# Kernel optimization log

Hardware: AMD Instinct MI355X
Metric: run time of the kernel (lower is better)

## Reference

```python
import jax, jax.numpy as jnp
import numpy as np

VOCAB = 78
EMBED = 8
HIDDEN = 256
BATCH = 512
SEQ = 512


def _lstm_layer(x, Wih, Whh, bih, bhh):
    # x: [B, T, in_dim]; Wih: [4H, in_dim]; Whh: [4H, H]
    B, T, _ = x.shape
    H = Whh.shape[1]
    # Precompute input projections for all timesteps: [T, B, 4H]
    xg = (jnp.einsum('bti,gi->btg', x, Wih) + bih + bhh).transpose(1, 0, 2)

    def step(carry, xg_t):
        h, c = carry
        gates = xg_t + h @ Whh.T  # [B, 4H]
        i, f, g, o = jnp.split(gates, 4, axis=-1)  # PyTorch gate order i,f,g,o
        i = jax.nn.sigmoid(i)
        f = jax.nn.sigmoid(f)
        g = jnp.tanh(g)
        o = jax.nn.sigmoid(o)
        c = f * c + i * g
        h = o * jnp.tanh(c)
        return (h, c), h

    h0 = jnp.zeros((B, H), dtype=x.dtype)
    c0 = jnp.zeros((B, H), dtype=x.dtype)
    (_, _), hs = jax.lax.scan(step, (h0, c0), xg)
    return hs.transpose(1, 0, 2)  # [B, T, H]


def setup_inputs() -> dict:
    key = jax.random.key(0)
    ks = jax.random.split(key, 12)
    k = 1.0 / np.sqrt(HIDDEN)
    u = lambda kk, shp, bound=k: jax.random.uniform(kk, shp, jnp.float32, -bound, bound)
    return {
        'x': jax.random.randint(ks[0], (BATCH, SEQ), 0, VOCAB),
        'E': jax.random.normal(ks[1], (VOCAB, EMBED), jnp.float32),
        'Wih0': u(ks[2], (4 * HIDDEN, EMBED)),
        'Whh0': u(ks[3], (4 * HIDDEN, HIDDEN)),
        'bih0': u(ks[4], (4 * HIDDEN,)),
        'bhh0': u(ks[5], (4 * HIDDEN,)),
        'Wih1': u(ks[6], (4 * HIDDEN, HIDDEN)),
        'Whh1': u(ks[7], (4 * HIDDEN, HIDDEN)),
        'bih1': u(ks[8], (4 * HIDDEN,)),
        'bhh1': u(ks[9], (4 * HIDDEN,)),
        'Wfc': u(ks[10], (VOCAB, HIDDEN)),
        'bfc': u(ks[11], (VOCAB,)),
    }


def reference(x, E, Wih0, Whh0, bih0, bhh0, Wih1, Whh1, bih1, bhh1, Wfc, bfc):
    E = E.at[0].set(0.0)  # padding_idx=0
    h = E[x]  # [B, T, EMBED]
    h = _lstm_layer(h, Wih0, Whh0, bih0, bhh0)
    # dropout=0.2 between layers is inactive in eval mode
    h = _lstm_layer(h, Wih1, Whh1, bih1, bhh1)
    return h[:, -1, :] @ Wfc.T + bfc  # [B, VOCAB]
```

## Files before the change

### kernel.cpp

```cpp
#include <hip/hip_runtime.h>
#include <hip/hip_bf16.h>

#define VOCAB 78
#define EMBED 8
#define HID 256
#define BATCH 512
#define SEQ 512
#define G4H 1024

#define GB 8
#define GH 16
#define BS 64
#define HS 16

typedef short bf16x8 __attribute__((ext_vector_type(8)));
typedef float f32x4 __attribute__((ext_vector_type(4)));
typedef unsigned long long u64;

#define OFF_WHH0 0
#define OFF_WIH1 (512*1024)
#define OFF_WHH1 (1024*1024)
#define OFF_XG0  (1536*1024)
#define OFF_B1   (OFF_XG0 + 320*1024)
#define OFF_XT   (OFF_B1 + 4096)
#define OFF_H0   (OFF_XT + 1024*1024)
#define OFF_H1   (OFF_H0 + 512*1024)
#define OFF_H1F  (OFF_H1 + 512*1024)
#define OFF_CNT  (OFF_H1F + 512*1024)
#define WS_NEED  (OFF_CNT + 1024)

__device__ __forceinline__ float sigm(float x){ return 1.f/(1.f + __expf(-x)); }
__device__ __forceinline__ float tanh_f(float x){
  float e = __expf(-2.f * fabsf(x));
  float r = (1.f - e) / (1.f + e);
  return copysignf(r, x);
}
__device__ __forceinline__ unsigned short f2b(float x){
  unsigned u = __float_as_uint(x);
  unsigned r = (u + 0x7FFFu + ((u >> 16) & 1u)) >> 16;
  return (unsigned short)r;
}

__global__ void prep(const int* __restrict__ x, const float* __restrict__ E,
                     const float* __restrict__ Wih0, const float* __restrict__ Whh0,
                     const float* __restrict__ bih0, const float* __restrict__ bhh0,
                     const float* __restrict__ Wih1, const float* __restrict__ Whh1,
                     const float* __restrict__ bih1, const float* __restrict__ bhh1,
                     unsigned char* __restrict__ ws)
{
  unsigned short* Whh0b = (unsigned short*)(ws + OFF_WHH0);
  unsigned short* Wih1b = (unsigned short*)(ws + OFF_WIH1);
  unsigned short* Whh1b = (unsigned short*)(ws + OFF_WHH1);
  float* xg0 = (float*)(ws + OFF_XG0);
  float* b1  = (float*)(ws + OFF_B1);
  int*   xT  = (int*)(ws + OFF_XT);

  long id = (long)blockIdx.x * 256 + threadIdx.x;
  const long NW = 1024L * 256;
  if (id < NW) { Whh0b[id] = f2b(Whh0[id]); return; }
  id -= NW;
  if (id < NW) { Wih1b[id] = f2b(Wih1[id]); return; }
  id -= NW;
  if (id < NW) { Whh1b[id] = f2b(Whh1[id]); return; }
  id -= NW;
  if (id < (long)VOCAB*G4H) {
    int v = (int)(id / G4H), row = (int)(id % G4H);
    float s = bih0[row] + bhh0[row];
    if (v != 0) {
      #pragma unroll
      for (int e = 0; e < EMBED; e++) s += E[v*EMBED + e] * Wih0[row*EMBED + e];
    }
    xg0[id] = s; return;
  }
  id -= (long)VOCAB*G4H;
  if (id < (long)SEQ*BATCH) {
    int t = (int)(id / BATCH), b = (int)(id % BATCH);
    xT[t*BATCH + b] = x[b*SEQ + t]; return;
  }
  id -= (long)SEQ*BATCH;
  if (id < G4H) { b1[id] = bih1[id] + bhh1[id]; return; }
  id -= G4H;
  if (id < 262144) { ((unsigned*)(ws + OFF_H0))[id] = 0u; return; }
  id -= 262144;
  if (id < 256) { ((unsigned*)(ws + OFF_CNT))[id] = 0u; }
}

__global__ __launch_bounds__(256, 1) void lstm_sync(unsigned char* __restrict__ ws)
{
  const unsigned short* Wg = (const unsigned short*)(ws + OFF_WHH0);
  const float* xg0 = (const float*)(ws + OFF_XG0);
  const float* b1  = (const float*)(ws + OFF_B1);
  const int*   xT  = (const int*)(ws + OFF_XT);
  unsigned short* h0g = (unsigned short*)(ws + OFF_H0);
  unsigned short* h1g = (unsigned short*)(ws + OFF_H1);
  float* h1f = (float*)(ws + OFF_H1F);

  __shared__ __align__(16) unsigned char smem[3*32768 + 64*48];
  unsigned char* wlds = smem;
  unsigned char* hb   = smem + 3*32768;

  const int tid = threadIdx.x;
  const int m = tid >> 6, l = tid & 63, lc = l & 15, lq = l >> 4;
  const int gb = blockIdx.x & 7, gh = blockIdx.x >> 3;
  const int B0 = gb * BS, J = gh * HS;
  const int brow0 = B0 + m*16;

  unsigned* cA = (unsigned*)(ws + OFF_CNT) + gb*16;
  unsigned* cB = cA + 1;

  for (int idx = tid; idx < 3*64*32; idx += 256) {
    int mat = idx >> 11;
    int rem = idx & 2047;
    int cw  = rem >> 5;
    int c16 = rem & 31;
    int g = cw >> 4, r16 = cw & 15;
    int grow = g*256 + J + r16;
    bf16x8 v = *(const bf16x8*)(Wg + (size_t)mat*262144 + (size_t)grow*256 + c16*8);
    *(bf16x8*)(wlds + mat*32768 + cw*512 + ((c16*16) ^ ((cw&7)<<4))) = v;
  }

  float bias1v[4];
  #pragma unroll
  for (int g = 0; g < 4; g++) bias1v[g] = b1[g*256 + J + lc];

  int wb[3][4];
  const int swz = (lc & 7) << 4;
  #pragma unroll
  for (int g = 0; g < 4; g++) {
    int cw = g*16 + lc;
    wb[0][g] = 0*32768 + cw*512;
    wb[1][g] = 1*32768 + cw*512;
    wb[2][g] = 2*32768 + cw*512;
  }
  __syncthreads();

  float c0[4] = {0,0,0,0}, c1[4] = {0,0,0,0};
  u64 xret = 0;

#define MM(acc, a, mat)                                                          \
  _Pragma("unroll") for (int kt = 0; kt < 8; kt++) {                             \
    _Pragma("unroll") for (int g = 0; g < 4; g++) {                              \
      bf16x8 bfr = *(const bf16x8*)(wlds + wb[mat][g] + ((kt*64 + lq*16) ^ swz));\
      acc[g] = __builtin_amdgcn_mfma_f32_16x16x32_bf16(a[kt], bfr, acc[g], 0,0,0);\
    } }

  #pragma unroll 1
  for (int k = 0; k <= SEQ; ++k) {
    const int pk = k & 1, pkm1 = pk ^ 1;

    __builtin_amdgcn_sched_barrier(0);
    asm volatile("" ::: "memory");

    bf16x8 a0[8];
    { const u64* hp = (const u64*)(h0g + (size_t)pkm1*131072 + (size_t)(brow0+lc)*256 + lq*8);
      #pragma unroll
      for (int kt = 0; kt < 8; kt++) {
        union { u64 q[2]; bf16x8 v; } u;
        u.q[0] = __hip_atomic_load(hp + kt*8 + 0, __ATOMIC_RELAXED, __HIP_MEMORY_SCOPE_SYSTEM);
        u.q[1] = __hip_atomic_load(hp + kt*8 + 1, __ATOMIC_RELAXED, __HIP_MEMORY_SCOPE_SYSTEM);
        a0[kt] = u.v;
      } }
    bf16x8 a1[8];
    if (k >= 1) {
      const u64* hp = (const u64*)(h1g + (size_t)pk*131072 + (size_t)(brow0+lc)*256 + lq*8);
      #pragma unroll
      for (int kt = 0; kt < 8; kt++) {
        union { u64 q[2]; bf16x8 v; } u;
        u.q[0] = __hip_atomic_load(hp + kt*8 + 0, __ATOMIC_RELAXED, __HIP_MEMORY_SCOPE_SYSTEM);
        u.q[1] = __hip_atomic_load(hp + kt*8 + 1, __ATOMIC_RELAXED, __HIP_MEMORY_SCOPE_SYSTEM);
        a1[kt] = u.v;
      }
    }

    if (k < SEQ) {
      float xg[4][4];
      #pragma unroll
      for (int r = 0; r < 4; r++) {
        int tok = xT[k*BATCH + brow0 + lq*4 + r];
        const float* tr = xg0 + (size_t)tok*G4H + J + lc;
        #pragma unroll
        for (int g = 0; g < 4; g++) xg[g][r] = tr[g*256];
      }
      f32x4 acc0[4] = {{0,0,0,0},{0,0,0,0},{0,0,0,0},{0,0,0,0}};
      MM(acc0, a0, 0);
      #pragma unroll
      for (int r = 0; r < 4; r++) {
        float gi = sigm (acc0[0][r] + xg[0][r]);
        float gf = sigm (acc0[1][r] + xg[1][r]);
        float gg = tanh_f(acc0[2][r] + xg[2][r]);
        float go = sigm (acc0[3][r] + xg[3][r]);
        float c = gf*c0[r] + gi*gg;  c0[r] = c;
        *(unsigned short*)(hb + (m*16 + lq*4 + r)*48 + lc*2) = f2b(go * tanh_f(c));
      }
      __syncthreads();
      { u64 pv = *(const u64*)(hb + (tid>>2)*48 + (tid&3)*8);
        u64* dp = (u64*)(h0g + (size_t)pk*131072 + (size_t)(B0 + (tid>>2))*256 + J + (tid&3)*4);
        xret ^= __hip_atomic_exchange(dp, pv, __ATOMIC_RELAXED, __HIP_MEMORY_SCOPE_AGENT); }
      asm volatile("" ::: "memory");
      __builtin_amdgcn_sched_barrier(0);
      __syncthreads();
      if (tid == 0)
        __hip_atomic_fetch_add(cA, 1u, __ATOMIC_RELAXED, __HIP_MEMORY_SCOPE_AGENT);
    }

    if (k >= 1) {
      f32x4 acc2[4];
      #pragma unroll
      for (int g = 0; g < 4; g++) { f32x4 v = {bias1v[g],bias1v[g],bias1v[g],bias1v[g]}; acc2[g] = v; }
      MM(acc2, a0, 1);
      MM(acc2, a1, 2);
      #pragma unroll
      for (int r = 0; r < 4; r++) {
        float gi = sigm (acc2[0][r]);
        float gf = sigm (acc2[1][r]);
        float gg = tanh_f(acc2[2][r]);
        float go = sigm (acc2[3][r]);
        float c = gf*c1[r] + gi*gg;  c1[r] = c;
        float h = go * tanh_f(c);
        *(unsigned short*)(hb + (m*16 + lq*4 + r)*48 + lc*2) = f2b(h);
        if (k == SEQ) h1f[(size_t)(brow0 + lq*4 + r)*256 + J + lc] = h;
      }
      __syncthreads();
      { u64 pv = *(const u64*)(hb + (tid>>2)*48 + (tid&3)*8);
        u64* dp = (u64*)(h1g + (size_t)pkm1*131072 + (size_t)(B0 + (tid>>2))*256 + J + (tid&3)*4);
        xret ^= __hip_atomic_exchange(dp, pv, __ATOMIC_RELAXED, __HIP_MEMORY_SCOPE_AGENT); }
      asm volatile("" ::: "memory");
      __builtin_amdgcn_sched_barrier(0);
      __syncthreads();
      if (tid == 0)
        __hip_atomic_fetch_add(cB, 1u, __ATOMIC_RELAXED, __HIP_MEMORY_SCOPE_AGENT);
    }

    if (k < SEQ) {
      if (tid == 0) {
        unsigned needA = 16u * (unsigned)(k + 1);
        unsigned needB = 16u * (unsigned)k;
        while (1) {
          u64 cv = __hip_atomic_load((u64*)cA, __ATOMIC_RELAXED, __HIP_MEMORY_SCOPE_AGENT);
          if ((unsigned)cv >= needA && (unsigned)(cv >> 32) >= needB) break;
          __builtin_amdgcn_s_sleep(1);
        }
      }
      __syncthreads();
    }
  }
#undef MM
  asm volatile("" :: "v"(xret));
}

__global__ void fc_kernel(const unsigned char* __restrict__ ws,
                          const float* __restrict__ Wfc, const float* __restrict__ bfc,
                          float* __restrict__ out)
{
  int b = blockIdx.x, v = threadIdx.x;
  if (v >= VOCAB) return;
  const float* h = (const float*)(ws + OFF_H1F) + (size_t)b*HID;
  const float* w = Wfc + (size_t)v*HID;
  float s = bfc[v];
  #pragma unroll 4
  for (int k = 0; k < HID; k += 4)
    s += h[k]*w[k] + h[k+1]*w[k+1] + h[k+2]*w[k+2] + h[k+3]*w[k+3];
  out[(size_t)b*VOCAB + v] = s;
}

extern "C" void kernel_launch(void* const* d_in, const int* in_sizes, int n_in,
                              void* d_out, int out_size, void* d_ws, size_t ws_size,
                              hipStream_t stream) {
  const int*   x    = (const int*)  d_in[0];
  const float* E    = (const float*)d_in[1];
  const float* Wih0 = (const float*)d_in[2];
  const float* Whh0 = (const float*)d_in[3];
  const float* bih0 = (const float*)d_in[4];
  const float* bhh0 = (const float*)d_in[5];
  const float* Wih1 = (const float*)d_in[6];
  const float* Whh1 = (const float*)d_in[7];
  const float* bih1 = (const float*)d_in[8];
  const float* bhh1 = (const float*)d_in[9];
  const float* Wfc  = (const float*)d_in[10];
  const float* bfc  = (const float*)d_in[11];
  unsigned char* ws = (unsigned char*)d_ws;

  prep<<<5437, 256, 0, stream>>>(x, E, Wih0, Whh0, bih0, bhh0, Wih1, Whh1, bih1, bhh1, ws);
  lstm_sync<<<GB*GH, 256, 0, stream>>>(ws);
  fc_kernel<<<BATCH, 128, 0, stream>>>(ws, Wfc, bfc, (float*)d_out);
}
```

Measured before the change: 4.384 ms.

## Split hidden units across 32 blocks per batch group with a single step counter

Each batch group is now spread over 32 blocks that each own 8 hidden units instead of 16. The gate columns are packed two per MFMA tile, and the f and o gates are exchanged across lanes with shuffles. The two per-layer counters and their barriers are merged into one counter incremented once per step, and h tiles are written straight to global memory from per-wave LDS without a block-wide sync. The aim is to halve per-block MFMA and LDS weight work per step and cut the number of block barriers, at the cost of twice as many blocks taking part in each group's spin-wait, half the lanes idling in the activation math, and the extra shuffles.

```diff
diff --git a/kernel.cpp b/kernel.cpp
--- a/kernel.cpp
+++ b/kernel.cpp
@@ -9,9 +9,9 @@
 #define G4H 1024
 
 #define GB 8
-#define GH 16
+#define GH 32
 #define BS 64
-#define HS 16
+#define HS 8
 
 typedef short bf16x8 __attribute__((ext_vector_type(8)));
 typedef float f32x4 __attribute__((ext_vector_type(4)));
@@ -95,9 +95,9 @@
   unsigned short* h1g = (unsigned short*)(ws + OFF_H1);
   float* h1f = (float*)(ws + OFF_H1F);
 
-  __shared__ __align__(16) unsigned char smem[3*32768 + 64*48];
+  __shared__ __align__(16) unsigned char smem[49152 + 1024];
   unsigned char* wlds = smem;
-  unsigned char* hb   = smem + 3*32768;
+  unsigned char* hb   = smem + 49152;
 
   const int tid = threadIdx.x;
   const int m = tid >> 6, l = tid & 63, lc = l & 15, lq = l >> 4;
@@ -105,43 +105,39 @@
   const int B0 = gb * BS, J = gh * HS;
   const int brow0 = B0 + m*16;
 
-  unsigned* cA = (unsigned*)(ws + OFF_CNT) + gb*16;
-  unsigned* cB = cA + 1;
-
-  for (int idx = tid; idx < 3*64*32; idx += 256) {
-    int mat = idx >> 11;
-    int rem = idx & 2047;
+  unsigned* cnt = (unsigned*)(ws + OFF_CNT) + gb*16;
+
+  for (int idx = tid; idx < 3*2*16*32; idx += 256) {
+    int mat = idx >> 10;
+    int rem = idx & 1023;
     int cw  = rem >> 5;
     int c16 = rem & 31;
-    int g = cw >> 4, r16 = cw & 15;
-    int grow = g*256 + J + r16;
+    int n = cw >> 4, i = cw & 15;
+    int grow = (2*n + (i>>3))*256 + J + (i&7);
     bf16x8 v = *(const bf16x8*)(Wg + (size_t)mat*262144 + (size_t)grow*256 + c16*8);
-    *(bf16x8*)(wlds + mat*32768 + cw*512 + ((c16*16) ^ ((cw&7)<<4))) = v;
-  }
-
-  float bias1v[4];
+    *(bf16x8*)(wlds + mat*16384 + cw*512 + ((c16*16) ^ ((i&7)<<4))) = v;
+  }
+
+  float biasv[2];
   #pragma unroll
-  for (int g = 0; g < 4; g++) bias1v[g] = b1[g*256 + J + lc];
-
-  int wb[3][4];
+  for (int n = 0; n < 2; n++) biasv[n] = b1[(2*n + (lc>>3))*256 + J + (lc&7)];
+
+  int wb[3][2];
   const int swz = (lc & 7) << 4;
   #pragma unroll
-  for (int g = 0; g < 4; g++) {
-    int cw = g*16 + lc;
-    wb[0][g] = 0*32768 + cw*512;
-    wb[1][g] = 1*32768 + cw*512;
-    wb[2][g] = 2*32768 + cw*512;
-  }
+  for (int mat = 0; mat < 3; mat++)
+    #pragma unroll
+    for (int n = 0; n < 2; n++) wb[mat][n] = mat*16384 + (n*16 + lc)*512;
   __syncthreads();
 
   float c0[4] = {0,0,0,0}, c1[4] = {0,0,0,0};
   u64 xret = 0;
 
-#define MM(acc, a, mat)                                                          \
-  _Pragma("unroll") for (int kt = 0; kt < 8; kt++) {                             \
-    _Pragma("unroll") for (int g = 0; g < 4; g++) {                              \
-      bf16x8 bfr = *(const bf16x8*)(wlds + wb[mat][g] + ((kt*64 + lq*16) ^ swz));\
-      acc[g] = __builtin_amdgcn_mfma_f32_16x16x32_bf16(a[kt], bfr, acc[g], 0,0,0);\
+#define MM(acc, a, mat)                                                            \
+  _Pragma("unroll") for (int kt = 0; kt < 8; kt++) {                               \
+    _Pragma("unroll") for (int n = 0; n < 2; n++) {                                \
+      bf16x8 bfr = *(const bf16x8*)(wlds + wb[mat][n] + ((kt*64 + lq*16) ^ swz));  \
+      acc[n] = __builtin_amdgcn_mfma_f32_16x16x32_bf16(a[kt], bfr, acc[n], 0,0,0); \
     } }
 
   #pragma unroll 1
@@ -174,72 +170,87 @@
 
     if (k < SEQ) {
       float xg[4][4];
+      if (lc < 8) {
+        #pragma unroll
+        for (int r = 0; r < 4; r++) {
+          int tok = xT[k*BATCH + brow0 + lq*4 + r];
+          const float* tr = xg0 + (size_t)tok*G4H + J + lc;
+          #pragma unroll
+          for (int g = 0; g < 4; g++) xg[g][r] = tr[g*256];
+        }
+      }
+      f32x4 acc0[2] = {{0,0,0,0},{0,0,0,0}};
+      MM(acc0, a0, 0);
+      float fpre[4], opre[4];
       #pragma unroll
       for (int r = 0; r < 4; r++) {
-        int tok = xT[k*BATCH + brow0 + lq*4 + r];
-        const float* tr = xg0 + (size_t)tok*G4H + J + lc;
+        fpre[r] = __shfl_xor(acc0[0][r], 8, 64);
+        opre[r] = __shfl_xor(acc0[1][r], 8, 64);
+      }
+      if (lc < 8) {
         #pragma unroll
-        for (int g = 0; g < 4; g++) xg[g][r] = tr[g*256];
-      }
-      f32x4 acc0[4] = {{0,0,0,0},{0,0,0,0},{0,0,0,0},{0,0,0,0}};
-      MM(acc0, a0, 0);
-      #pragma unroll
-      for (int r = 0; r < 4; r++) {
-        float gi = sigm (acc0[0][r] + xg[0][r]);
-        float gf = sigm (acc0[1][r] + xg[1][r]);
-        float gg = tanh_f(acc0[2][r] + xg[2][r]);
-        float go = sigm (acc0[3][r] + xg[3][r]);
-        float c = gf*c0[r] + gi*gg;  c0[r] = c;
-        *(unsigned short*)(hb + (m*16 + lq*4 + r)*48 + lc*2) = f2b(go * tanh_f(c));
-      }
-      __syncthreads();
-      { u64 pv = *(const u64*)(hb + (tid>>2)*48 + (tid&3)*8);
-        u64* dp = (u64*)(h0g + (size_t)pk*131072 + (size_t)(B0 + (tid>>2))*256 + J + (tid&3)*4);
-        xret ^= __hip_atomic_exchange(dp, pv, __ATOMIC_RELAXED, __HIP_MEMORY_SCOPE_AGENT); }
+        for (int r = 0; r < 4; r++) {
+          float gi = sigm (acc0[0][r] + xg[0][r]);
+          float gf = sigm (fpre[r]    + xg[1][r]);
+          float gg = tanh_f(acc0[1][r] + xg[2][r]);
+          float go = sigm (opre[r]    + xg[3][r]);
+          float c = gf*c0[r] + gi*gg;  c0[r] = c;
+          *(unsigned short*)(hb + m*256 + (lq*4 + r)*16 + lc*2) = f2b(go * tanh_f(c));
+        }
+      }
+      if (l < 32) {
+        int row = l >> 1, half = l & 1;
+        u64 pv = *(const u64*)(hb + m*256 + row*16 + half*8);
+        u64* dp = (u64*)(h0g + (size_t)pk*131072 + (size_t)(B0 + m*16 + row)*256 + J + half*4);
+        xret ^= __hip_atomic_exchange(dp, pv, __ATOMIC_RELAXED, __HIP_MEMORY_SCOPE_AGENT);
+      }
       asm volatile("" ::: "memory");
       __builtin_amdgcn_sched_barrier(0);
-      __syncthreads();
-      if (tid == 0)
-        __hip_atomic_fetch_add(cA, 1u, __ATOMIC_RELAXED, __HIP_MEMORY_SCOPE_AGENT);
     }
 
     if (k >= 1) {
-      f32x4 acc2[4];
-      #pragma unroll
-      for (int g = 0; g < 4; g++) { f32x4 v = {bias1v[g],bias1v[g],bias1v[g],bias1v[g]}; acc2[g] = v; }
+      f32x4 acc2[2];
+      #pragma unroll
+      for (int n = 0; n < 2; n++) { f32x4 v = {biasv[n],biasv[n],biasv[n],biasv[n]}; acc2[n] = v; }
       MM(acc2, a0, 1);
       MM(acc2, a1, 2);
+      float fpre[4], opre[4];
       #pragma unroll
       for (int r = 0; r < 4; r++) {
-        float gi = sigm (acc2[0][r]);
-        float gf = sigm (acc2[1][r]);
-        float gg = tanh_f(acc2[2][r]);
-        float go = sigm (acc2[3][r]);
-        float c = gf*c1[r] + gi*gg;  c1[r] = c;
-        float h = go * tanh_f(c);
-        *(unsigned short*)(hb + (m*16 + lq*4 + r)*48 + lc*2) = f2b(h);
-        if (k == SEQ) h1f[(size_t)(brow0 + lq*4 + r)*256 + J + lc] = h;
-      }
-      __syncthreads();
-      { u64 pv = *(const u64*)(hb + (tid>>2)*48 + (tid&3)*8);
-        u64* dp = (u64*)(h1g + (size_t)pkm1*131072 + (size_t)(B0 + (tid>>2))*256 + J + (tid&3)*4);
-        xret ^= __hip_atomic_exchange(dp, pv, __ATOMIC_RELAXED, __HIP_MEMORY_SCOPE_AGENT); }
+        fpre[r] = __shfl_xor(acc2[0][r], 8, 64);
+        opre[r] = __shfl_xor(acc2[1][r], 8, 64);
+      }
+      if (lc < 8) {
+        #pragma unroll
+        for (int r = 0; r < 4; r++) {
+          float gi = sigm (acc2[0][r]);
+          float gf = sigm (fpre[r]);
+          float gg = tanh_f(acc2[1][r]);
+          float go = sigm (opre[r]);
+          float c = gf*c1[r] + gi*gg;  c1[r] = c;
+          float h = go * tanh_f(c);
+          *(unsigned short*)(hb + m*256 + (lq*4 + r)*16 + lc*2) = f2b(h);
+          if (k == SEQ) h1f[(size_t)(brow0 + lq*4 + r)*256 + J + lc] = h;
+        }
+      }
+      if (l < 32) {
+        int row = l >> 1, half = l & 1;
+        u64 pv = *(const u64*)(hb + m*256 + row*16 + half*8);
+        u64* dp = (u64*)(h1g + (size_t)pkm1*131072 + (size_t)(B0 + m*16 + row)*256 + J + half*4);
+        xret ^= __hip_atomic_exchange(dp, pv, __ATOMIC_RELAXED, __HIP_MEMORY_SCOPE_AGENT);
+      }
       asm volatile("" ::: "memory");
       __builtin_amdgcn_sched_barrier(0);
-      __syncthreads();
-      if (tid == 0)
-        __hip_atomic_fetch_add(cB, 1u, __ATOMIC_RELAXED, __HIP_MEMORY_SCOPE_AGENT);
-    }
-
+    }
+
+    __syncthreads();
+    if (tid == 0)
+      __hip_atomic_fetch_add(cnt, 1u, __ATOMIC_RELAXED, __HIP_MEMORY_SCOPE_AGENT);
     if (k < SEQ) {
       if (tid == 0) {
-        unsigned needA = 16u * (unsigned)(k + 1);
-        unsigned needB = 16u * (unsigned)k;
-        while (1) {
-          u64 cv = __hip_atomic_load((u64*)cA, __ATOMIC_RELAXED, __HIP_MEMORY_SCOPE_AGENT);
-          if ((unsigned)cv >= needA && (unsigned)(cv >> 32) >= needB) break;
+        unsigned need = 32u * (unsigned)(k + 1);
+        while (__hip_atomic_load(cnt, __ATOMIC_RELAXED, __HIP_MEMORY_SCOPE_AGENT) < need)
           __builtin_amdgcn_s_sleep(1);
-        }
       }
       __syncthreads();
     }
```

Result: no change. 4.298 ms (-2.0%).
